# Optimization experiments

Hardware: AMD Instinct MI355X
Metric: run time of the kernel (lower is better)

Reference implementation:

```python
import jax, jax.numpy as jnp
import numpy as np
import math

N, NCB, DIM, CB = 16384, 16, 4, 1024
LOG2 = math.log(2.0)


def setup_inputs() -> dict:
    key = jax.random.key(0)
    k1, k2, k3 = jax.random.split(key, 3)
    x = jax.random.normal(k1, (N, NCB, DIM), jnp.float32)
    # codebook init ~ N(0, 1/sqrt(cb_dim)) as in the torch module
    codebook = jax.random.normal(k2, (NCB, CB, DIM), jnp.float32) / math.sqrt(DIM)
    logits = 0.01 * jax.random.normal(k3, (NCB, CB), jnp.float32)
    lmbda = jnp.asarray(128.0, jnp.float32)
    return {"x": x, "codebook": codebook, "logits": logits, "lmbda": lmbda}


def reference(x, codebook, logits, lmbda):
    # Unconditional entropy model: log2 pmf from softmax over logits
    log2_pmf_u = jax.nn.log_softmax(logits, axis=-1) / (-LOG2)      # (ncb, cb)
    rate_bias = log2_pmf_u / lmbda                                   # (ncb, cb)

    # Squared L2 distance: (N, ncb, cb)
    dist = ((x * x).sum(-1)[..., None]
            + (codebook * codebook).sum(-1)[None]
            - 2.0 * jnp.einsum('nad,acd->nac', x, codebook))
    dist = dist + rate_bias[None]

    index = jnp.argmin(dist, axis=-1)                                # (N, ncb)
    cb_idx = jnp.arange(NCB)[None, :]                                # (1, ncb)

    # one-hot @ codebook == gather of selected codewords
    x_hat = codebook[cb_idx, index]                                  # (N, ncb, dim)
    # (one_hot * log2_pmf_u).sum() == sum of selected log2 probs
    rate_uem = log2_pmf_u[cb_idx, index].sum()

    rate_cem = jnp.zeros((), x.dtype)
    prior_dist = jnp.zeros((1,), x.dtype)
    param_bit = jnp.zeros((1,), x.dtype)
    return (x_hat, rate_uem, rate_cem, prior_dist, param_bit)
```

## Files before the change

kernel.cpp:

```cpp
#include <hip/hip_runtime.h>

#define N_ROWS 16384
#define NCB    16
#define CB     1024

__global__ void zero_tail_kernel(float* p) {
    int t = threadIdx.x;
    if (t < 4) p[t] = 0.0f;
}

__global__ __launch_bounds__(256) void ecvq_kernel(
    const float4* __restrict__ x,
    const float4* __restrict__ cbook,
    const float*  __restrict__ logits,
    const float*  __restrict__ lmbda_p,
    float4* __restrict__ xhat,
    float*  __restrict__ tail)
{
    __shared__ float4 s_cb[CB];
    __shared__ float  s_cnb[CB];
    __shared__ float  s_l2u[CB];
    __shared__ float  sredA[4];
    __shared__ float  sredB[4];

    const int a     = blockIdx.x;
    const int chunk = blockIdx.y;
    const int t     = threadIdx.x;

    float  l[4];
    float4 w4[4];
    float  m = -INFINITY;
#pragma unroll
    for (int r = 0; r < 4; ++r) {
        int i = t + 256 * r;
        l[r]    = logits[a * CB + i];
        w4[r]   = cbook[a * CB + i];
        s_cb[i] = w4[r];
        m = fmaxf(m, l[r]);
    }
#pragma unroll
    for (int off = 32; off >= 1; off >>= 1) m = fmaxf(m, __shfl_down(m, off, 64));
    if ((t & 63) == 0) sredA[t >> 6] = m;
    __syncthreads();
    const float gmax = fmaxf(fmaxf(sredA[0], sredA[1]), fmaxf(sredA[2], sredA[3]));

    float s = 0.f;
#pragma unroll
    for (int r = 0; r < 4; ++r) s += __expf(l[r] - gmax);
#pragma unroll
    for (int off = 32; off >= 1; off >>= 1) s += __shfl_down(s, off, 64);
    if ((t & 63) == 0) sredB[t >> 6] = s;
    __syncthreads();
    const float lse       = gmax + __logf(sredB[0] + sredB[1] + sredB[2] + sredB[3]);
    const float inv_lmbda = 1.0f / lmbda_p[0];
    const float INV_LN2   = 1.4426950408889634f;
#pragma unroll
    for (int r = 0; r < 4; ++r) {
        int i = t + 256 * r;
        float v  = (lse - l[r]) * INV_LN2;
        s_l2u[i] = v;
        float cc = w4[r].x * w4[r].x + w4[r].y * w4[r].y
                 + w4[r].z * w4[r].z + w4[r].w * w4[r].w;
        s_cnb[i] = cc + v * inv_lmbda;
    }
    __syncthreads();

    const int nbase = chunk * 1024 + t;
    float4 xm2[4];
#pragma unroll
    for (int r = 0; r < 4; ++r) {
        float4 xv = x[(nbase + 256 * r) * NCB + a];
        xm2[r] = make_float4(-2.f * xv.x, -2.f * xv.y, -2.f * xv.z, -2.f * xv.w);
    }

    float dmin[4] = {INFINITY, INFINITY, INFINITY, INFINITY};
    int   imin[4] = {0, 0, 0, 0};
#pragma unroll 4
    for (int c = 0; c < CB; ++c) {
        const float4 w    = s_cb[c];
        const float  base = s_cnb[c];
#pragma unroll
        for (int r = 0; r < 4; ++r) {
            float d = fmaf(xm2[r].x, w.x, base);
            d = fmaf(xm2[r].y, w.y, d);
            d = fmaf(xm2[r].z, w.z, d);
            d = fmaf(xm2[r].w, w.w, d);
            bool lt = d < dmin[r];
            dmin[r] = lt ? d : dmin[r];
            imin[r] = lt ? c : imin[r];
        }
    }

    float rsum = 0.f;
#pragma unroll
    for (int r = 0; r < 4; ++r) {
        xhat[(nbase + 256 * r) * NCB + a] = s_cb[imin[r]];
        rsum += s_l2u[imin[r]];
    }
#pragma unroll
    for (int off = 32; off >= 1; off >>= 1) rsum += __shfl_down(rsum, off, 64);
    __shared__ float wsum[4];
    if ((t & 63) == 0) wsum[t >> 6] = rsum;
    __syncthreads();
    if (t == 0) atomicAdd(&tail[0], wsum[0] + wsum[1] + wsum[2] + wsum[3]);
}

extern "C" void kernel_launch(void* const* d_in, const int* in_sizes, int n_in,
                              void* d_out, int out_size, void* d_ws, size_t ws_size,
                              hipStream_t stream) {
    (void)in_sizes; (void)n_in; (void)out_size; (void)d_ws; (void)ws_size;
    const float4* x      = (const float4*)d_in[0];
    const float4* cbook  = (const float4*)d_in[1];
    const float*  logits = (const float*)d_in[2];
    const float*  lmbda  = (const float*)d_in[3];

    float* out  = (float*)d_out;
    float* tail = out + (size_t)N_ROWS * NCB * 4;

    zero_tail_kernel<<<1, 64, 0, stream>>>(tail);

    dim3 grid(NCB, N_ROWS / 1024);
    ecvq_kernel<<<grid, 256, 0, stream>>>(x, cbook, logits, lmbda,
                                          (float4*)d_out, tail);
}
```

Before: 128.4 us.

## Split codebook prep into separate kernel and use one row per thread

Moves the softmax/log2-pmf and codeword-norm computation into a prep kernel that writes to workspace, so each search block no longer redoes it. The search kernel now processes one row per thread over a grid four times larger, and reads codewords and norms straight from global memory (uniform addresses, scalar/cached loads) in place of LDS. The aim is more parallelism and less redundant prep work. The cost is an extra launch and less reuse of each codeword load across rows.

```diff
diff --git a/kernel.cpp b/kernel.cpp
--- a/kernel.cpp
+++ b/kernel.cpp
@@ -3,39 +3,29 @@
 #define N_ROWS 16384
 #define NCB    16
 #define CB     1024
+#define TPB    256
 
 __global__ void zero_tail_kernel(float* p) {
     int t = threadIdx.x;
     if (t < 4) p[t] = 0.0f;
 }
 
-__global__ __launch_bounds__(256) void ecvq_kernel(
-    const float4* __restrict__ x,
+__global__ __launch_bounds__(256) void prep_kernel(
     const float4* __restrict__ cbook,
     const float*  __restrict__ logits,
     const float*  __restrict__ lmbda_p,
-    float4* __restrict__ xhat,
-    float*  __restrict__ tail)
+    float* __restrict__ ws_cnb,
+    float* __restrict__ ws_l2u)
 {
-    __shared__ float4 s_cb[CB];
-    __shared__ float  s_cnb[CB];
-    __shared__ float  s_l2u[CB];
-    __shared__ float  sredA[4];
-    __shared__ float  sredB[4];
+    const int a = blockIdx.x;
+    const int t = threadIdx.x;
+    __shared__ float sredA[4], sredB[4];
 
-    const int a     = blockIdx.x;
-    const int chunk = blockIdx.y;
-    const int t     = threadIdx.x;
-
-    float  l[4];
-    float4 w4[4];
-    float  m = -INFINITY;
+    float l[4];
+    float m = -INFINITY;
 #pragma unroll
     for (int r = 0; r < 4; ++r) {
-        int i = t + 256 * r;
-        l[r]    = logits[a * CB + i];
-        w4[r]   = cbook[a * CB + i];
-        s_cb[i] = w4[r];
+        l[r] = logits[a * CB + t + 256 * r];
         m = fmaxf(m, l[r]);
     }
 #pragma unroll
@@ -51,64 +41,85 @@
     for (int off = 32; off >= 1; off >>= 1) s += __shfl_down(s, off, 64);
     if ((t & 63) == 0) sredB[t >> 6] = s;
     __syncthreads();
-    const float lse       = gmax + __logf(sredB[0] + sredB[1] + sredB[2] + sredB[3]);
-    const float inv_lmbda = 1.0f / lmbda_p[0];
-    const float INV_LN2   = 1.4426950408889634f;
+    const float lse   = gmax + __logf(sredB[0] + sredB[1] + sredB[2] + sredB[3]);
+    const float inv_l = 1.0f / lmbda_p[0];
+    const float INV_LN2 = 1.4426950408889634f;
 #pragma unroll
     for (int r = 0; r < 4; ++r) {
         int i = t + 256 * r;
+        float4 w = cbook[a * CB + i];
         float v  = (lse - l[r]) * INV_LN2;
-        s_l2u[i] = v;
-        float cc = w4[r].x * w4[r].x + w4[r].y * w4[r].y
-                 + w4[r].z * w4[r].z + w4[r].w * w4[r].w;
-        s_cnb[i] = cc + v * inv_lmbda;
+        ws_l2u[a * CB + i] = v;
+        ws_cnb[a * CB + i] = w.x * w.x + w.y * w.y + w.z * w.z + w.w * w.w
+                           + v * inv_l;
     }
+}
+
+__global__ __launch_bounds__(TPB) void ecvq_kernel(
+    const float4* __restrict__ x,
+    const float4* __restrict__ cbook,
+    const float*  __restrict__ ws_cnb,
+    const float*  __restrict__ ws_l2u,
+    float4* __restrict__ xhat,
+    float*  __restrict__ tail)
+{
+    __shared__ float4 s_cb[CB];
+    __shared__ float  s_l2u[CB];
+
+    const int a     = blockIdx.x;
+    const int chunk = blockIdx.y;
+    const int t     = threadIdx.x;
+
+#pragma unroll
+    for (int r = 0; r < CB / TPB; ++r) {
+        int i = t + TPB * r;
+        s_cb[i]  = cbook[a * CB + i];
+        s_l2u[i] = ws_l2u[a * CB + i];
+    }
+
+    const int n = chunk * TPB + t;
+    const float4 xv = x[n * NCB + a];
+    const float4 xm2 = make_float4(-2.f * xv.x, -2.f * xv.y,
+                                   -2.f * xv.z, -2.f * xv.w);
     __syncthreads();
 
-    const int nbase = chunk * 1024 + t;
-    float4 xm2[4];
-#pragma unroll
-    for (int r = 0; r < 4; ++r) {
-        float4 xv = x[(nbase + 256 * r) * NCB + a];
-        xm2[r] = make_float4(-2.f * xv.x, -2.f * xv.y, -2.f * xv.z, -2.f * xv.w);
+    const float4* __restrict__ cb  = cbook  + a * CB;
+    const float*  __restrict__ cnb = ws_cnb + a * CB;
+
+    float dmin = INFINITY;
+    int   imin = 0;
+#pragma unroll 8
+    for (int c = 0; c < CB; ++c) {
+        const float4 w = cb[c];
+        float d = xm2.x * w.x;
+        d = fmaf(xm2.y, w.y, d);
+        d = fmaf(xm2.z, w.z, d);
+        d = fmaf(xm2.w, w.w, d);
+        d += cnb[c];
+        bool lt = d < dmin;
+        dmin = lt ? d : dmin;
+        imin = lt ? c : imin;
     }
 
-    float dmin[4] = {INFINITY, INFINITY, INFINITY, INFINITY};
-    int   imin[4] = {0, 0, 0, 0};
-#pragma unroll 4
-    for (int c = 0; c < CB; ++c) {
-        const float4 w    = s_cb[c];
-        const float  base = s_cnb[c];
-#pragma unroll
-        for (int r = 0; r < 4; ++r) {
-            float d = fmaf(xm2[r].x, w.x, base);
-            d = fmaf(xm2[r].y, w.y, d);
-            d = fmaf(xm2[r].z, w.z, d);
-            d = fmaf(xm2[r].w, w.w, d);
-            bool lt = d < dmin[r];
-            dmin[r] = lt ? d : dmin[r];
-            imin[r] = lt ? c : imin[r];
-        }
-    }
-
-    float rsum = 0.f;
-#pragma unroll
-    for (int r = 0; r < 4; ++r) {
-        xhat[(nbase + 256 * r) * NCB + a] = s_cb[imin[r]];
-        rsum += s_l2u[imin[r]];
-    }
+    xhat[n * NCB + a] = s_cb[imin];
+    float rsum = s_l2u[imin];
 #pragma unroll
     for (int off = 32; off >= 1; off >>= 1) rsum += __shfl_down(rsum, off, 64);
-    __shared__ float wsum[4];
+    __shared__ float wsum[TPB / 64];
     if ((t & 63) == 0) wsum[t >> 6] = rsum;
     __syncthreads();
-    if (t == 0) atomicAdd(&tail[0], wsum[0] + wsum[1] + wsum[2] + wsum[3]);
+    if (t == 0) {
+        float tot = wsum[0];
+#pragma unroll
+        for (int w = 1; w < TPB / 64; ++w) tot += wsum[w];
+        atomicAdd(&tail[0], tot);
+    }
 }
 
 extern "C" void kernel_launch(void* const* d_in, const int* in_sizes, int n_in,
                               void* d_out, int out_size, void* d_ws, size_t ws_size,
                               hipStream_t stream) {
-    (void)in_sizes; (void)n_in; (void)out_size; (void)d_ws; (void)ws_size;
+    (void)in_sizes; (void)n_in; (void)out_size; (void)ws_size;
     const float4* x      = (const float4*)d_in[0];
     const float4* cbook  = (const float4*)d_in[1];
     const float*  logits = (const float*)d_in[2];
@@ -117,9 +128,13 @@
     float* out  = (float*)d_out;
     float* tail = out + (size_t)N_ROWS * NCB * 4;
 
+    float* ws_cnb = (float*)d_ws;
+    float* ws_l2u = ws_cnb + NCB * CB;
+
     zero_tail_kernel<<<1, 64, 0, stream>>>(tail);
+    prep_kernel<<<NCB, 256, 0, stream>>>(cbook, logits, lmbda, ws_cnb, ws_l2u);
 
-    dim3 grid(NCB, N_ROWS / 1024);
-    ecvq_kernel<<<grid, 256, 0, stream>>>(x, cbook, logits, lmbda,
+    dim3 grid(NCB, N_ROWS / TPB);
+    ecvq_kernel<<<grid, TPB, 0, stream>>>(x, cbook, ws_cnb, ws_l2u,
                                           (float4*)d_out, tail);
 }
```

Result: slower. 140.7 us (+9.6%).
